# Kernel optimization log

Hardware: AMD Instinct MI355X
Metric: run time of the kernel (lower is better)

Reference implementation:

```python
import jax, jax.numpy as jnp
from jax import lax
import numpy as np

B, H, W, C = 16, 128, 256, 64
D = 12            # local_max_disp // stride
H_OUT, W_OUT = 1024, 2048


def setup_inputs() -> dict:
    key = jax.random.key(0)
    ks = jax.random.split(key, 8)
    feat_l = jax.random.normal(ks[0], (B, H, W, C), dtype=jnp.float32)
    feat_r = jax.random.normal(ks[1], (B, H, W, C), dtype=jnp.float32)
    def conv_w(k, shape):
        fan_in = shape[0] * shape[1] * shape[2] * shape[3]
        return jax.random.normal(k, shape, dtype=jnp.float32) / np.sqrt(fan_in)
    return {
        'feat_l': feat_l, 'feat_r': feat_r,
        'w0': conv_w(ks[2], (3, 3, 3, 1, 4)), 'b0': jnp.zeros((4,), jnp.float32),
        'w1': conv_w(ks[3], (3, 3, 3, 4, 4)), 'b1': jnp.zeros((4,), jnp.float32),
        'w2': conv_w(ks[4], (3, 3, 3, 4, 4)), 'b2': jnp.zeros((4,), jnp.float32),
        'w3': conv_w(ks[5], (3, 3, 3, 4, 4)), 'b3': jnp.zeros((4,), jnp.float32),
        'wf': conv_w(ks[6], (3, 3, 3, 4, 1)), 'bf': jnp.zeros((1,), jnp.float32),
    }


def _cost_volume(feat_l, feat_r, max_disp, stride):
    # For disparity i: cost[:, :, w, i] = sum_c |L[b,h,w,c] - R[b,h,w-i,c]| for w >= i,
    # and sum_c |L[b,h,w,c]| for w < i (which equals diff against a zero-padded shift of R).
    planes = []
    for i in range(0, max_disp, stride):
        if i == 0:
            r_shift = feat_r
        else:
            r_shift = jnp.pad(feat_r[:, :, :-i, :], ((0, 0), (0, 0), (i, 0), (0, 0)))
        planes.append(jnp.sum(jnp.abs(feat_l - r_shift), axis=-1))
    return jnp.stack(planes, axis=-1)  # [B,H,W,D]


def _conv3d(x, w, b):
    # x: [B,H,W,D,C_in], w: [3,3,3,C_in,C_out]
    y = lax.conv_general_dilated(x, w, (1, 1, 1), 'SAME',
                                 dimension_numbers=('NHWDC', 'HWDIO', 'NHWDC'))
    return y + b


def reference(feat_l, feat_r, w0, b0, w1, b1, w2, b2, w3, b3, wf, bf):
    cost = _cost_volume(feat_l, feat_r, D, 1)          # [B,H,W,D]
    x = cost[..., None]                                 # [B,H,W,D,1]
    x = jax.nn.relu(_conv3d(x, w0, b0))
    x = jax.nn.relu(_conv3d(x, w1, b1))
    x = jax.nn.relu(_conv3d(x, w2, b2))
    x = jax.nn.relu(_conv3d(x, w3, b3))
    x = _conv3d(x, wf, bf)                              # [B,H,W,D,1]
    cost = x[..., 0]                                    # [B,H,W,D]
    sm = jax.nn.softmax(-cost, axis=-1)
    disp = jnp.arange(D, dtype=jnp.float32)
    pred = jnp.sum(sm * disp, axis=-1, keepdims=True)   # [B,H,W,1]
    out = jax.image.resize(pred, (pred.shape[0], H_OUT, W_OUT, 1), method='bilinear')
    return out
```

## Files before the change

### kernel.cpp

```cpp
#include <hip/hip_runtime.h>
#include <cstddef>

#define BB   16
#define HHY  128
#define WWX  256
#define CC   64
#define DDp  12
#define HOUT 1024
#define WOUT 2048

typedef _Float16 hf;
typedef __fp16 h2 __attribute__((ext_vector_type(2)));

__device__ __forceinline__ h2 u2h(unsigned u) { return __builtin_bit_cast(h2, u); }
__device__ __forceinline__ unsigned pkrtz(float a, float b) {
  return __builtin_bit_cast(unsigned, __builtin_amdgcn_cvt_pkrtz(a, b));
}

#if defined(__has_builtin)
#if __has_builtin(__builtin_amdgcn_fdot2)
#define FDOT2(a, b, c) __builtin_amdgcn_fdot2((a), (b), (c), false)
#endif
#endif
#ifndef FDOT2
#define FDOT2(a, b, c) ((float)(a)[0] * (float)(b)[0] + (float)(a)[1] * (float)(b)[1] + (c))
#endif

__global__ __launch_bounds__(256) void prep_k(const float* __restrict__ w1,
                                              const float* __restrict__ w2,
                                              const float* __restrict__ w3,
                                              const float* __restrict__ wf,
                                              hf* __restrict__ o) {
  const int t = threadIdx.x;
  for (int i = t; i < 432; i += 256) {
    const int t27 = i >> 4;
    const int ci = (i >> 2) & 3;
    const int co = i & 3;
    const int dst = (t27 * 4 + co) * 4 + ci;
    o[dst]       = (hf)w1[i];
    o[432 + dst] = (hf)w2[i];
    o[864 + dst] = (hf)w3[i];
  }
  for (int i = t; i < 108; i += 256) o[1296 + i] = (hf)wf[i];
}

#define CCH 16
#define LST 20

__global__ __launch_bounds__(256) void cost_volume_k(const float* __restrict__ L,
                                                     const float* __restrict__ R,
                                                     float* __restrict__ cost) {
  __shared__ float lsR[WWX * LST];
  const int t = threadIdx.x;
  const int h = blockIdx.x;
  const int b = blockIdx.y;
  const size_t rowbase = ((size_t)(b * HHY + h)) * WWX;
  const float* Lrow = L + rowbase * CC;
  const float* Rrow = R + rowbase * CC;

  float acc[DDp];
#pragma unroll
  for (int d = 0; d < DDp; ++d) acc[d] = 0.f;

  const int ph = (h ^ (b << 1)) & 3;
#pragma unroll
  for (int p = 0; p < 4; ++p) {
    const int c0 = ((p + ph) & 3) * CCH;
    __syncthreads();
#pragma unroll
    for (int j = 0; j < 4; ++j) {
      const int i = t + 256 * j;
      const int w = i >> 2;
      const int r4 = (i & 3) << 2;
      *(float4*)(&lsR[w * LST + r4]) =
          *(const float4*)(Rrow + (size_t)w * CC + c0 + r4);
    }
    __syncthreads();

    float l[CCH];
#pragma unroll
    for (int k = 0; k < CCH / 4; ++k)
      ((float4*)l)[k] = *(const float4*)(Lrow + (size_t)t * CC + c0 + 4 * k);

    float sl = 0.f;
#pragma unroll
    for (int k = 0; k < CCH; ++k) sl += fabsf(l[k]);

#pragma unroll
    for (int d = 0; d < DDp; ++d) {
      if (t >= d) {
        const float* rp = &lsR[(t - d) * LST];
        float a = 0.f;
#pragma unroll
        for (int k = 0; k < CCH / 4; ++k) {
          const float4 r4 = *(const float4*)(rp + 4 * k);
          a += fabsf(l[4 * k + 0] - r4.x) + fabsf(l[4 * k + 1] - r4.y) +
               fabsf(l[4 * k + 2] - r4.z) + fabsf(l[4 * k + 3] - r4.w);
        }
        acc[d] += a;
      } else {
        acc[d] += sl;
      }
    }
  }

  float* cp = cost + (rowbase + t) * DDp;
#pragma unroll
  for (int d = 0; d < DDp; d += 4)
    *(float4*)(cp + d) = make_float4(acc[d], acc[d + 1], acc[d + 2], acc[d + 3]);
}

__global__ __launch_bounds__(256) void conv0_k(const float* __restrict__ x,
                                               const float* __restrict__ wt,
                                               const float* __restrict__ bs,
                                               hf* __restrict__ y) {
  constexpr int S = 20;
  __shared__ float ls[WWX * S];
  const int t = threadIdx.x;
  const int id = blockIdx.x;
  const int h = ((id & 7) << 4) | ((id >> 3) & 15);
  const int b = id >> 7;

  float acc[DDp][4];
#pragma unroll
  for (int co = 0; co < 4; ++co) {
    const float bv = bs[co];
#pragma unroll
    for (int d = 0; d < DDp; ++d) acc[d][co] = bv;
  }

#pragma unroll
  for (int kh = 0; kh < 3; ++kh) {
    const int hh = h + kh - 1;
    if (hh < 0 || hh >= HHY) continue;

    __syncthreads();
    const float* xr = x + ((size_t)(b * HHY + hh) * WWX) * DDp;
#pragma unroll
    for (int j = 0; j < 3; ++j) {
      const int fi4 = t + 256 * j;
      const int w_ = fi4 / 3;
      const int k_ = fi4 - w_ * 3;
      *(float4*)(&ls[w_ * S + k_ * 4]) = ((const float4*)xr)[fi4];
    }
    __syncthreads();

#pragma unroll
    for (int kw = 0; kw < 3; ++kw) {
      const int ww = t + kw - 1;
      if (ww < 0 || ww >= WWX) continue;
      const float* lp = &ls[ww * S];

      const float* wp = wt + (size_t)(kh * 3 + kw) * 12;
      float wr[12];
#pragma unroll
      for (int i = 0; i < 12; ++i) wr[i] = wp[i];

      float v[DDp];
#pragma unroll
      for (int k = 0; k < 3; ++k)
        ((float4*)v)[k] = *(const float4*)(lp + 4 * k);
#pragma unroll
      for (int vo = 0; vo < DDp; ++vo)
#pragma unroll
        for (int kd = 0; kd < 3; ++kd) {
          const int d = vo + 1 - kd;
          if (d < 0 || d >= DDp) continue;
#pragma unroll
          for (int co = 0; co < 4; ++co)
            acc[d][co] += v[vo] * wr[kd * 4 + co];
        }
    }
  }

  unsigned ov[DDp * 2];
#pragma unroll
  for (int d = 0; d < DDp; ++d) {
    ov[d * 2]     = pkrtz(fmaxf(acc[d][0], 0.f), fmaxf(acc[d][1], 0.f));
    ov[d * 2 + 1] = pkrtz(fmaxf(acc[d][2], 0.f), fmaxf(acc[d][3], 0.f));
  }
  uint4* yp = (uint4*)(y + ((size_t)(b * HHY + h) * WWX + t) * (DDp * 4));
#pragma unroll
  for (int i = 0; i < 6; ++i) yp[i] = ((uint4*)ov)[i];
}

template <int COUT, bool FUSE_SM>
__global__ __launch_bounds__(256) void convh_k(const hf* __restrict__ x,
                                               const hf* __restrict__ wh,
                                               const float* __restrict__ bs,
                                               void* __restrict__ yv) {
  constexpr int DCH = DDp * 4;
  constexpr int SU  = 26;
  __shared__ unsigned lsu[WWX * SU];

  const int t = threadIdx.x;
  const int id = blockIdx.x;
  const int h = ((id & 7) << 4) | ((id >> 3) & 15);
  const int b = id >> 7;

  float acc[DDp][COUT];
#pragma unroll
  for (int co = 0; co < COUT; ++co) {
    const float bv = bs[co];
#pragma unroll
    for (int d = 0; d < DDp; ++d) acc[d][co] = bv;
  }

  const unsigned* whu = (const unsigned*)wh;

#pragma unroll
  for (int kh = 0; kh < 3; ++kh) {
    const int hh = h + kh - 1;
    if (hh < 0 || hh >= HHY) continue;

    __syncthreads();
    const uint4* xr = (const uint4*)(x + (size_t)(b * HHY + hh) * WWX * DCH);
#pragma unroll
    for (int j = 0; j < 6; ++j) {
      const int fi4 = t + 256 * j;
      const int w_ = fi4 / 6;
      const int k_ = fi4 - w_ * 6;
      const uint4 v = xr[fi4];
      unsigned* dst = &lsu[w_ * SU + k_ * 4];
      *(uint2*)(dst)     = make_uint2(v.x, v.y);
      *(uint2*)(dst + 2) = make_uint2(v.z, v.w);
    }
    __syncthreads();

#pragma unroll
    for (int kw = 0; kw < 3; ++kw) {
      const int ww = t + kw - 1;
      if (ww < 0 || ww >= WWX) continue;

      unsigned w01[3][COUT], w23[3][COUT];
      const int tap3 = (kh * 3 + kw) * 3;
#pragma unroll
      for (int kd = 0; kd < 3; ++kd)
#pragma unroll
        for (int co = 0; co < COUT; ++co) {
          const int u0 = ((tap3 + kd) * COUT + co) * 2;
          w01[kd][co] = whu[u0];
          w23[kd][co] = whu[u0 + 1];
        }

      const unsigned* lp = &lsu[ww * SU];
#pragma unroll
      for (int vo = 0; vo < DDp; ++vo) {
        const uint2 xu = *(const uint2*)(lp + vo * 2);
        const h2 x01 = u2h(xu.x), x23 = u2h(xu.y);
#pragma unroll
        for (int kd = 0; kd < 3; ++kd) {
          const int d = vo + 1 - kd;
          if (d < 0 || d >= DDp) continue;
#pragma unroll
          for (int co = 0; co < COUT; ++co)
            acc[d][co] = FDOT2(x01, u2h(w01[kd][co]),
                         FDOT2(x23, u2h(w23[kd][co]), acc[d][co]));
        }
      }
    }
  }

  if constexpr (FUSE_SM) {
    float* y = (float*)yv;
    float mn = acc[0][0];
#pragma unroll
    for (int d = 1; d < DDp; ++d) mn = fminf(mn, acc[d][0]);
    float s = 0.f, sw = 0.f;
#pragma unroll
    for (int d = 0; d < DDp; ++d) {
      const float e = __expf(mn - acc[d][0]);
      s += e;
      sw += e * (float)d;
    }
    y[(size_t)(b * HHY + h) * WWX + t] = sw / s;
  } else {
    hf* y = (hf*)yv;
    unsigned ov[DDp * 2];
#pragma unroll
    for (int d = 0; d < DDp; ++d) {
      ov[d * 2]     = pkrtz(fmaxf(acc[d][0], 0.f), fmaxf(acc[d][1 % COUT], 0.f));
      ov[d * 2 + 1] = pkrtz(fmaxf(acc[d][2 % COUT], 0.f), fmaxf(acc[d][3 % COUT], 0.f));
    }
    uint4* yp = (uint4*)(y + ((size_t)(b * HHY + h) * WWX + t) * DCH);
#pragma unroll
    for (int i = 0; i < 6; ++i) yp[i] = ((uint4*)ov)[i];
  }
}

__global__ __launch_bounds__(256) void resize4_k(const float* __restrict__ pred,
                                                 float* __restrict__ out) {
  const int idx = blockIdx.x * 256 + threadIdx.x;
  const int xg = idx & 511;
  const int y = (idx >> 9) & 1023;
  const int b = idx >> 19;

  const int parity = xg & 1;
  const int m = xg >> 1;
  const int x0 = m - 1 + parity;
  const int x0c = max(x0, 0);
  const int x1c = min(x0 + 1, WWX - 1);
  const float wx0 = (parity ? 0.0625f : 0.5625f);

  const int py = y & 7;
  const int my = y >> 3;
  const int y0 = my - 1 + (py >= 4 ? 1 : 0);
  const float wy = (py >= 4) ? 0.0625f + (py - 4) * 0.125f : 0.5625f + py * 0.125f;
  const int y0c = max(y0, 0);
  const int y1c = min(y0 + 1, HHY - 1);

  const float* pb = pred + (size_t)b * HHY * WWX;
  const float a = pb[y0c * WWX + x0c];
  const float bv = pb[y0c * WWX + x1c];
  const float c = pb[y1c * WWX + x0c];
  const float d = pb[y1c * WWX + x1c];

  const float top0 = a + (bv - a) * wx0;
  const float bot0 = c + (d - c) * wx0;
  const float dtop = (bv - a) * 0.125f;
  const float dbot = (d - c) * 0.125f;

  float4 o;
  o.x = top0 + wy * (bot0 - top0);
  o.y = (top0 + dtop) + wy * ((bot0 + dbot) - (top0 + dtop));
  o.z = (top0 + 2.f * dtop) + wy * ((bot0 + 2.f * dbot) - (top0 + 2.f * dtop));
  o.w = (top0 + 3.f * dtop) + wy * ((bot0 + 3.f * dbot) - (top0 + 3.f * dtop));

  *(float4*)(out + (size_t)idx * 4) = o;
}

extern "C" void kernel_launch(void* const* d_in, const int* in_sizes, int n_in,
                              void* d_out, int out_size, void* d_ws, size_t ws_size,
                              hipStream_t stream) {
  const float* feat_l = (const float*)d_in[0];
  const float* feat_r = (const float*)d_in[1];
  const float* w0 = (const float*)d_in[2];
  const float* b0 = (const float*)d_in[3];
  const float* w1 = (const float*)d_in[4];
  const float* b1 = (const float*)d_in[5];
  const float* w2 = (const float*)d_in[6];
  const float* b2 = (const float*)d_in[7];
  const float* w3 = (const float*)d_in[8];
  const float* b3 = (const float*)d_in[9];
  const float* wf = (const float*)d_in[10];
  const float* bf = (const float*)d_in[11];
  float* out = (float*)d_out;

  char* ws = (char*)d_ws;
  hf*    A  = (hf*)ws;
  hf*    Bf = (hf*)(ws + 50331648);
  float* C  = (float*)(ws + 100663296);
  float* P  = (float*)(ws + 125829120);
  hf*    Wh = (hf*)(ws + 127926272);

  dim3 blk(256);
  prep_k<<<dim3(1), blk, 0, stream>>>(w1, w2, w3, wf, Wh);
  cost_volume_k<<<dim3(HHY, BB), blk, 0, stream>>>(feat_l, feat_r, C);
  conv0_k<<<dim3(HHY * BB), blk, 0, stream>>>(C, w0, b0, A);
  convh_k<4, false><<<dim3(HHY * BB), blk, 0, stream>>>(A,  Wh,        b1, Bf);
  convh_k<4, false><<<dim3(HHY * BB), blk, 0, stream>>>(Bf, Wh + 432,  b2, A);
  convh_k<4, false><<<dim3(HHY * BB), blk, 0, stream>>>(A,  Wh + 864,  b3, Bf);
  convh_k<1, true ><<<dim3(HHY * BB), blk, 0, stream>>>(Bf, Wh + 1296, bf, P);

  const int ngroups = BB * HOUT * (WOUT / 4);
  resize4_k<<<dim3(ngroups / 256), blk, 0, stream>>>(P, out);
}
```

Before: 316.5 us.

## Compute cost volume in packed fp16 with abs-dot and full-channel LDS tile

```diff
diff --git a/kernel.cpp b/kernel.cpp
--- a/kernel.cpp
+++ b/kernel.cpp
@@ -25,6 +25,12 @@
 #ifndef FDOT2
 #define FDOT2(a, b, c) ((float)(a)[0] * (float)(b)[0] + (float)(a)[1] * (float)(b)[1] + (c))
 #endif
+
+__device__ __forceinline__ float adot(unsigned lu, unsigned ru, float c) {
+  const h2 d = u2h(lu) - u2h(ru);
+  const unsigned au = __builtin_bit_cast(unsigned, d) & 0x7FFF7FFFu;
+  return FDOT2(u2h(au), u2h(0x3C003C00u), c);
+}
 
 __global__ __launch_bounds__(256) void prep_k(const float* __restrict__ w1,
                                               const float* __restrict__ w2,
@@ -44,13 +50,12 @@
   for (int i = t; i < 108; i += 256) o[1296 + i] = (hf)wf[i];
 }
 
-#define CCH 16
-#define LST 20
+#define RSTRIDE 36
 
 __global__ __launch_bounds__(256) void cost_volume_k(const float* __restrict__ L,
                                                      const float* __restrict__ R,
                                                      float* __restrict__ cost) {
-  __shared__ float lsR[WWX * LST];
+  __shared__ unsigned lsR[WWX * RSTRIDE];
   const int t = threadIdx.x;
   const int h = blockIdx.x;
   const int b = blockIdx.y;
@@ -58,49 +63,47 @@
   const float* Lrow = L + rowbase * CC;
   const float* Rrow = R + rowbase * CC;
 
+#pragma unroll
+  for (int j = 0; j < 16; ++j) {
+    const int fi = t + 256 * j;
+    const int w = fi >> 4;
+    const int f4 = fi & 15;
+    const float4 v = *(const float4*)(Rrow + (size_t)w * CC + 4 * f4);
+    *(uint2*)(&lsR[w * RSTRIDE + f4 * 2]) =
+        make_uint2(pkrtz(v.x, v.y), pkrtz(v.z, v.w));
+  }
+
+  unsigned lh[32];
+#pragma unroll
+  for (int k = 0; k < 16; ++k) {
+    const float4 v = *(const float4*)(Lrow + (size_t)t * CC + 4 * k);
+    lh[2 * k]     = pkrtz(v.x, v.y);
+    lh[2 * k + 1] = pkrtz(v.z, v.w);
+  }
+
+  float sl = 0.f;
+#pragma unroll
+  for (int i = 0; i < 32; ++i) sl = adot(lh[i], 0u, sl);
+
+  __syncthreads();
+
   float acc[DDp];
 #pragma unroll
-  for (int d = 0; d < DDp; ++d) acc[d] = 0.f;
-
-  const int ph = (h ^ (b << 1)) & 3;
-#pragma unroll
-  for (int p = 0; p < 4; ++p) {
-    const int c0 = ((p + ph) & 3) * CCH;
-    __syncthreads();
-#pragma unroll
-    for (int j = 0; j < 4; ++j) {
-      const int i = t + 256 * j;
-      const int w = i >> 2;
-      const int r4 = (i & 3) << 2;
-      *(float4*)(&lsR[w * LST + r4]) =
-          *(const float4*)(Rrow + (size_t)w * CC + c0 + r4);
-    }
-    __syncthreads();
-
-    float l[CCH];
-#pragma unroll
-    for (int k = 0; k < CCH / 4; ++k)
-      ((float4*)l)[k] = *(const float4*)(Lrow + (size_t)t * CC + c0 + 4 * k);
-
-    float sl = 0.f;
-#pragma unroll
-    for (int k = 0; k < CCH; ++k) sl += fabsf(l[k]);
-
-#pragma unroll
-    for (int d = 0; d < DDp; ++d) {
-      if (t >= d) {
-        const float* rp = &lsR[(t - d) * LST];
-        float a = 0.f;
-#pragma unroll
-        for (int k = 0; k < CCH / 4; ++k) {
-          const float4 r4 = *(const float4*)(rp + 4 * k);
-          a += fabsf(l[4 * k + 0] - r4.x) + fabsf(l[4 * k + 1] - r4.y) +
-               fabsf(l[4 * k + 2] - r4.z) + fabsf(l[4 * k + 3] - r4.w);
-        }
-        acc[d] += a;
-      } else {
-        acc[d] += sl;
+  for (int d = 0; d < DDp; ++d) {
+    if (t >= d) {
+      const unsigned* rp = &lsR[(t - d) * RSTRIDE];
+      float a = 0.f;
+#pragma unroll
+      for (int k = 0; k < 8; ++k) {
+        const uint4 r = *(const uint4*)(rp + 4 * k);
+        a = adot(lh[4 * k + 0], r.x, a);
+        a = adot(lh[4 * k + 1], r.y, a);
+        a = adot(lh[4 * k + 2], r.z, a);
+        a = adot(lh[4 * k + 3], r.w, a);
       }
+      acc[d] = a;
+    } else {
+      acc[d] = sl;
     }
   }
 
```

Result: faster. 299.5 us (-5.4%).

## Stage full R row in LDS via direct global-to-LDS loads with XOR swizzle

Applied to the files above, without the earlier changes.

```diff
diff --git a/kernel.cpp b/kernel.cpp
--- a/kernel.cpp
+++ b/kernel.cpp
@@ -44,13 +44,12 @@
   for (int i = t; i < 108; i += 256) o[1296 + i] = (hf)wf[i];
 }
 
-#define CCH 16
-#define LST 20
+#define ZROWB (WWX * CC)
 
 __global__ __launch_bounds__(256) void cost_volume_k(const float* __restrict__ L,
                                                      const float* __restrict__ R,
                                                      float* __restrict__ cost) {
-  __shared__ float lsR[WWX * LST];
+  __shared__ __align__(16) unsigned lsR[WWX * CC + 64];
   const int t = threadIdx.x;
   const int h = blockIdx.x;
   const int b = blockIdx.y;
@@ -58,49 +57,48 @@
   const float* Lrow = L + rowbase * CC;
   const float* Rrow = R + rowbase * CC;
 
+  {
+    const int wv = t >> 6, ln = t & 63;
+    const unsigned* gR = (const unsigned*)Rrow;
+#pragma unroll
+    for (int i = 0; i < 16; ++i) {
+      const int s  = (wv * 16 + i) * 64 + ln;
+      const int w  = s >> 4;
+      const int jj = s & 15;
+      const int gj = jj ^ (w & 15);
+      __builtin_amdgcn_global_load_lds(gR + (size_t)w * CC + gj * 4,
+                                       &lsR[(wv * 16 + i) * 256], 16, 0, 0);
+    }
+  }
+
+  if (t < 64) lsR[ZROWB + t] = 0u;
+
+  float4 l4[16];
+#pragma unroll
+  for (int k = 0; k < 16; ++k)
+    l4[k] = *(const float4*)(Lrow + (size_t)t * CC + 4 * k);
+
+  __syncthreads();
+
+  int rb[DDp], rx[DDp];
+#pragma unroll
+  for (int d = 0; d < DDp; ++d) {
+    rb[d] = (t >= d) ? ((t - d) << 6) : ZROWB;
+    rx[d] = (t >= d) ? ((t - d) & 15) : 0;
+  }
+
   float acc[DDp];
 #pragma unroll
   for (int d = 0; d < DDp; ++d) acc[d] = 0.f;
 
-  const int ph = (h ^ (b << 1)) & 3;
-#pragma unroll
-  for (int p = 0; p < 4; ++p) {
-    const int c0 = ((p + ph) & 3) * CCH;
-    __syncthreads();
-#pragma unroll
-    for (int j = 0; j < 4; ++j) {
-      const int i = t + 256 * j;
-      const int w = i >> 2;
-      const int r4 = (i & 3) << 2;
-      *(float4*)(&lsR[w * LST + r4]) =
-          *(const float4*)(Rrow + (size_t)w * CC + c0 + r4);
-    }
-    __syncthreads();
-
-    float l[CCH];
-#pragma unroll
-    for (int k = 0; k < CCH / 4; ++k)
-      ((float4*)l)[k] = *(const float4*)(Lrow + (size_t)t * CC + c0 + 4 * k);
-
-    float sl = 0.f;
-#pragma unroll
-    for (int k = 0; k < CCH; ++k) sl += fabsf(l[k]);
-
+#pragma unroll
+  for (int k = 0; k < 16; ++k) {
+    const float4 lv = l4[k];
 #pragma unroll
     for (int d = 0; d < DDp; ++d) {
-      if (t >= d) {
-        const float* rp = &lsR[(t - d) * LST];
-        float a = 0.f;
-#pragma unroll
-        for (int k = 0; k < CCH / 4; ++k) {
-          const float4 r4 = *(const float4*)(rp + 4 * k);
-          a += fabsf(l[4 * k + 0] - r4.x) + fabsf(l[4 * k + 1] - r4.y) +
-               fabsf(l[4 * k + 2] - r4.z) + fabsf(l[4 * k + 3] - r4.w);
-        }
-        acc[d] += a;
-      } else {
-        acc[d] += sl;
-      }
+      const float4 r = *(const float4*)&lsR[rb[d] + ((k ^ rx[d]) << 2)];
+      acc[d] += fabsf(lv.x - r.x) + fabsf(lv.y - r.y) +
+                fabsf(lv.z - r.z) + fabsf(lv.w - r.w);
     }
   }
 
```

Measured after the change: 327.5 us. 3.5% more time.
